# Kernel optimization log

Measured on AMD Instinct MI355X. Metric: run time of the kernel, lower is better.

## Reference

```python
import jax, jax.numpy as jnp
import numpy as np

GAMMA = 1.5
BN_EPS = 1e-5


def sparsemax(z):
    """Sparsemax along last axis (Martins & Astudillo, 2016)."""
    z = z - jnp.max(z, axis=-1, keepdims=True)
    z_sorted = -jnp.sort(-z, axis=-1)                      # descending sort
    z_cumsum = jnp.cumsum(z_sorted, axis=-1)
    k = jnp.arange(1, z.shape[-1] + 1, dtype=z.dtype)
    support = (z_sorted - (z_cumsum - 1.0) / k) > 0
    k_z = jnp.clip(jnp.sum(support, axis=-1, keepdims=True), 1, None).astype(z.dtype)
    idx = (k_z - 1.0).astype(jnp.int32)
    tau = (jnp.take_along_axis(z_cumsum, idx, axis=-1) - 1.0) / k_z
    return jnp.clip(z - tau, 0.0, None)


def setup_inputs() -> dict:
    key = jax.random.key(0)
    k1, k2 = jax.random.split(key)
    B, T, E, H = 32, 512, 512, 8
    x = jax.random.normal(k1, (B, T, E), dtype=jnp.float32)
    # torch Linear weight (out, in), kaiming-ish scale
    W = jax.random.normal(k2, (H, E, E), dtype=jnp.float32) / np.float32(np.sqrt(E))
    bn_weight = jnp.ones((H, E), dtype=jnp.float32)
    bn_bias = jnp.zeros((H, E), dtype=jnp.float32)
    return {"x": x, "W": W, "bn_weight": bn_weight, "bn_bias": bn_bias}


def reference(x, W, bn_weight, bn_bias):
    B, T, E = x.shape
    H = W.shape[0]
    gi = x.reshape(B * T, E)
    # all-head linear: y[n,o] = sum_i gi[n,i] * W[h,o,i]
    logits = jnp.einsum('ni,hoi->hno', gi, W)              # (H, B*T, E)
    # BatchNorm1d in training mode: batch stats over the B*T axis, biased var
    mean = jnp.mean(logits, axis=1, keepdims=True)
    var = jnp.var(logits, axis=1, keepdims=True)
    logits = (logits - mean) / jnp.sqrt(var + BN_EPS)
    logits = logits * bn_weight[:, None, :] + bn_bias[:, None, :]
    logits = logits.reshape(H, B, T, E)

    prior0 = jnp.ones((B, T, E), dtype=x.dtype)

    def step(prior, logits_h):
        mask_h = sparsemax(logits_h * prior)
        prior = prior * jnp.clip(GAMMA - mask_h, 0.0, None)
        return prior, mask_h

    _, masks = jax.lax.scan(step, prior0, logits)          # masks: (H, B, T, E)
    masked_xs = x[None, :, :, :] * masks                   # (H, B, T, E)
    return masked_xs, jnp.transpose(masks, (1, 0, 2, 3))   # (B, H, T, E)
```

## Files before the change

kernel.cpp:

```cpp
#include <hip/hip_runtime.h>
#include <stdint.h>

#define Hh 8
#define Bb 32
#define Tt 512
#define Ee 512
#define Nn 16384
#define GAMMA_ 1.5f
#define BN_EPS_ 1e-5f

typedef _Float16 f16x4 __attribute__((ext_vector_type(4)));
typedef _Float16 f16x8 __attribute__((ext_vector_type(8)));
typedef float    f32x4 __attribute__((ext_vector_type(4)));

__device__ __forceinline__ void async_ld16(void* lds, const void* g) {
    __builtin_amdgcn_global_load_lds(
        (const __attribute__((address_space(1))) void*)g,
        (__attribute__((address_space(3))) void*)lds, 16, 0, 0);
}

__device__ __forceinline__ float dpp_sum64(float v) {
    int t;
    t = __builtin_amdgcn_update_dpp(0, __float_as_int(v), 0x111, 0xf, 0xf, true);
    v += __int_as_float(t);
    t = __builtin_amdgcn_update_dpp(0, __float_as_int(v), 0x112, 0xf, 0xf, true);
    v += __int_as_float(t);
    t = __builtin_amdgcn_update_dpp(0, __float_as_int(v), 0x114, 0xf, 0xf, true);
    v += __int_as_float(t);
    t = __builtin_amdgcn_update_dpp(0, __float_as_int(v), 0x118, 0xf, 0xf, true);
    v += __int_as_float(t);
    t = __builtin_amdgcn_update_dpp(0, __float_as_int(v), 0x142, 0xf, 0xf, true);
    v += __int_as_float(t);
    t = __builtin_amdgcn_update_dpp(0, __float_as_int(v), 0x143, 0xf, 0xf, true);
    v += __int_as_float(t);
    return __int_as_float(__builtin_amdgcn_readlane(__float_as_int(v), 63));
}

__device__ __forceinline__ float dpp_max64(float v) {
    int t;
    t = __builtin_amdgcn_update_dpp(__float_as_int(v), __float_as_int(v), 0x111, 0xf, 0xf, false);
    v = fmaxf(v, __int_as_float(t));
    t = __builtin_amdgcn_update_dpp(__float_as_int(v), __float_as_int(v), 0x112, 0xf, 0xf, false);
    v = fmaxf(v, __int_as_float(t));
    t = __builtin_amdgcn_update_dpp(__float_as_int(v), __float_as_int(v), 0x114, 0xf, 0xf, false);
    v = fmaxf(v, __int_as_float(t));
    t = __builtin_amdgcn_update_dpp(__float_as_int(v), __float_as_int(v), 0x118, 0xf, 0xf, false);
    v = fmaxf(v, __int_as_float(t));
    t = __builtin_amdgcn_update_dpp(__float_as_int(v), __float_as_int(v), 0x142, 0xf, 0xf, false);
    v = fmaxf(v, __int_as_float(t));
    t = __builtin_amdgcn_update_dpp(__float_as_int(v), __float_as_int(v), 0x143, 0xf, 0xf, false);
    v = fmaxf(v, __int_as_float(t));
    return __int_as_float(__builtin_amdgcn_readlane(__float_as_int(v), 63));
}

__global__ __launch_bounds__(256) void cvt_kernel(const float* __restrict__ x,
                                                  const float* __restrict__ W,
                                                  _Float16* __restrict__ xh,
                                                  _Float16* __restrict__ wh,
                                                  float* __restrict__ sums) {
    const int NX = Bb * Tt * Ee;
    const int tid_g = blockIdx.x * 256 + threadIdx.x;
    int i = tid_g * 4;
    if (i < NX) {
        float4 v = *(const float4*)(x + i);
        f16x4 o = {(_Float16)v.x, (_Float16)v.y, (_Float16)v.z, (_Float16)v.w};
        *(f16x4*)(xh + i) = o;
    } else {
        int j = i - NX;
        float4 v = *(const float4*)(W + j);
        f16x4 o = {(_Float16)v.x, (_Float16)v.y, (_Float16)v.z, (_Float16)v.w};
        *(f16x4*)(wh + j) = o;
    }
    int zi = tid_g - (2621440 - 2048);
    if (zi >= 0) {
        float4 zz = {0.f, 0.f, 0.f, 0.f};
        ((float4*)sums)[zi] = zz;
    }
}

__global__ __launch_bounds__(512, 2) void gemm_kernel(const _Float16* __restrict__ A,
                                                      const _Float16* __restrict__ Bm,
                                                      _Float16* __restrict__ C,
                                                      float* __restrict__ sums,
                                                      float* __restrict__ sumsq) {
    __shared__ alignas(16) _Float16 As[2][256 * 32];
    __shared__ alignas(16) _Float16 Bs[2][256 * 32];
    const int id  = blockIdx.x;
    const int h   = id >> 7;
    const int rem = id & 127;
    const int mb  = (rem >> 1) * 256;
    const int nb  = (rem & 1) * 256;

    const int t    = threadIdx.x;
    const int lane = t & 63;
    const int w    = t >> 6;
    const int wrow = (w >> 2) * 128;
    const int wcol = (w & 3) * 64;
    const int quad = lane >> 4;
    const int l16  = lane & 15;

    const int kc = ((t & 3) - ((t >> 3) & 3)) & 3;
    const _Float16* Ap = A + (size_t)(mb + (t >> 2)) * Ee + kc * 8;
    const _Float16* Bp = Bm + (size_t)h * Ee * Ee + (size_t)(nb + (t >> 2)) * Ee + kc * 8;

    f32x4 acc[8][4] = {};

    async_ld16(&As[0][t * 8],        Ap);
    async_ld16(&As[0][4096 + t * 8], Ap + 128 * Ee);
    async_ld16(&Bs[0][t * 8],        Bp);
    async_ld16(&Bs[0][4096 + t * 8], Bp + 128 * Ee);

    const int so = ((quad + (l16 >> 1)) & 3) * 8;

    int buf = 0;
    for (int k0 = 0; k0 < Ee; k0 += 32) {
        __syncthreads();
        if (k0 + 32 < Ee) {
            int nx = buf ^ 1;
            async_ld16(&As[nx][t * 8],        Ap + k0 + 32);
            async_ld16(&As[nx][4096 + t * 8], Ap + 128 * Ee + k0 + 32);
            async_ld16(&Bs[nx][t * 8],        Bp + k0 + 32);
            async_ld16(&Bs[nx][4096 + t * 8], Bp + 128 * Ee + k0 + 32);
        }
        f16x8 b8[4];
#pragma unroll
        for (int nt = 0; nt < 4; ++nt)
            b8[nt] = *(const f16x8*)(&Bs[buf][(wcol + nt * 16 + l16) * 32 + so]);
#pragma unroll
        for (int mt = 0; mt < 8; ++mt) {
            f16x8 a8 = *(const f16x8*)(&As[buf][(wrow + mt * 16 + l16) * 32 + so]);
#pragma unroll
            for (int nt = 0; nt < 4; ++nt)
                acc[mt][nt] = __builtin_amdgcn_mfma_f32_16x16x32_f16(a8, b8[nt], acc[mt][nt], 0, 0, 0);
        }
        buf ^= 1;
    }

#pragma unroll
    for (int nt = 0; nt < 4; ++nt) {
        float sv = 0.f, ss = 0.f;
#pragma unroll
        for (int mt = 0; mt < 8; ++mt)
#pragma unroll
            for (int rr = 0; rr < 4; ++rr) { float v = acc[mt][nt][rr]; sv += v; ss += v * v; }
        sv += __shfl_xor(sv, 16, 64); sv += __shfl_xor(sv, 32, 64);
        ss += __shfl_xor(ss, 16, 64); ss += __shfl_xor(ss, 32, 64);
        if (quad == 0) {
            int col = nb + wcol + nt * 16 + l16;
            atomicAdd(&sums[h * Ee + col], sv);
            atomicAdd(&sumsq[h * Ee + col], ss);
        }
    }

    _Float16* Cp = C + (size_t)h * Nn * Ee;
#pragma unroll
    for (int mt = 0; mt < 8; ++mt)
#pragma unroll
        for (int rr = 0; rr < 4; ++rr) {
            int row = mb + wrow + mt * 16 + quad * 4 + rr;
            size_t off = (size_t)row * Ee + nb + wcol + l16;
#pragma unroll
            for (int nt = 0; nt < 4; ++nt)
                Cp[off + nt * 16] = (_Float16)acc[mt][nt][rr];
        }
}

__global__ __launch_bounds__(256) void stats_kernel(const float* __restrict__ sums,
                                                    const float* __restrict__ sumsq,
                                                    const float* __restrict__ bnw,
                                                    const float* __restrict__ bnb,
                                                    float* __restrict__ cA,
                                                    float* __restrict__ cB) {
    int i = blockIdx.x * 256 + threadIdx.x;
    float mean = sums[i] * (1.0f / Nn);
    float var  = sumsq[i] * (1.0f / Nn) - mean * mean;
    float inv  = rsqrtf(var + BN_EPS_);
    float a    = bnw[i] * inv;
    cA[i] = a;
    cB[i] = bnb[i] - mean * a;
}

__global__ __launch_bounds__(256) void rows_kernel(const float* __restrict__ x,
                                                   const _Float16* __restrict__ lg,
                                                   const float* __restrict__ cA,
                                                   const float* __restrict__ cB,
                                                   float* __restrict__ out) {
    const int n    = blockIdx.x * 4 + (threadIdx.x >> 6);
    const int lane = threadIdx.x & 63;
    const int e0   = lane * 4;
    const int bb   = n >> 9;
    const int tt   = n & 511;

    float xr[8], prior[8];
    {
        const float* xp = x + (size_t)n * Ee;
        float4 x0 = *(const float4*)(xp + e0);
        float4 x1 = *(const float4*)(xp + 256 + e0);
        xr[0]=x0.x; xr[1]=x0.y; xr[2]=x0.z; xr[3]=x0.w;
        xr[4]=x1.x; xr[5]=x1.y; xr[6]=x1.z; xr[7]=x1.w;
    }
#pragma unroll
    for (int j = 0; j < 8; ++j) prior[j] = 1.0f;

    float* omx = out;
    float* omk = out + (size_t)Hh * Nn * Ee;

    const _Float16* lrow = lg + (size_t)n * Ee;
    f16x4 l0 = *(const f16x4*)(lrow + e0);
    f16x4 l1 = *(const f16x4*)(lrow + 256 + e0);

#pragma unroll 1
    for (int h = 0; h < Hh; ++h) {
        f16x4 p0 = l0, p1 = l1;
        if (h + 1 < Hh) {
            const _Float16* lnx = lrow + (size_t)(h + 1) * Nn * Ee;
            p0 = *(const f16x4*)(lnx + e0);
            p1 = *(const f16x4*)(lnx + 256 + e0);
        }
        float z[8];
        {
            const float* ap = cA + h * Ee + e0;
            const float* bp = cB + h * Ee + e0;
            float4 a0 = *(const float4*)(ap);
            float4 b0 = *(const float4*)(bp);
            float4 a1 = *(const float4*)(ap + 256);
            float4 b1 = *(const float4*)(bp + 256);
            z[0] = ((float)l0[0] * a0.x + b0.x) * prior[0];
            z[1] = ((float)l0[1] * a0.y + b0.y) * prior[1];
            z[2] = ((float)l0[2] * a0.z + b0.z) * prior[2];
            z[3] = ((float)l0[3] * a0.w + b0.w) * prior[3];
            z[4] = ((float)l1[0] * a1.x + b1.x) * prior[4];
            z[5] = ((float)l1[1] * a1.y + b1.y) * prior[5];
            z[6] = ((float)l1[2] * a1.z + b1.z) * prior[6];
            z[7] = ((float)l1[3] * a1.w + b1.w) * prior[7];
        }

        float mx = z[0];
#pragma unroll
        for (int j = 1; j < 8; ++j) mx = fmaxf(mx, z[j]);
        float tau = dpp_max64(mx) - 1.0f;
        int cprev = -1;
#pragma unroll 1
        for (int it = 0; it < 64; ++it) {
            float s2 = 0.f;
            int cnt = 0;
#pragma unroll
            for (int j = 0; j < 8; ++j) {
                bool p = z[j] > tau;
                s2 += p ? z[j] : 0.0f;
                cnt += (int)__popcll(__ballot(p));
            }
            float S = dpp_sum64(s2);
            if (cnt == cprev) break;
            cprev = cnt;
            tau = (S - 1.0f) / (float)cnt;
        }

        size_t oxoff = ((size_t)h * Nn + n) * Ee + e0;
        size_t okoff = (((size_t)bb * Hh + h) * Tt + tt) * Ee + e0;
        f32x4 vx, vm;
#pragma unroll
        for (int j = 0; j < 4; ++j) {
            float m = fmaxf(z[j] - tau, 0.0f);
            prior[j] *= fmaxf(GAMMA_ - m, 0.0f);
            vm[j] = m; vx[j] = xr[j] * m;
        }
        __builtin_nontemporal_store(vx, (f32x4*)(omx + oxoff));
        __builtin_nontemporal_store(vm, (f32x4*)(omk + okoff));
#pragma unroll
        for (int j = 0; j < 4; ++j) {
            float m = fmaxf(z[4 + j] - tau, 0.0f);
            prior[4 + j] *= fmaxf(GAMMA_ - m, 0.0f);
            vm[j] = m; vx[j] = xr[4 + j] * m;
        }
        __builtin_nontemporal_store(vx, (f32x4*)(omx + oxoff + 256));
        __builtin_nontemporal_store(vm, (f32x4*)(omk + okoff + 256));
        l0 = p0; l1 = p1;
    }
}

extern "C" void kernel_launch(void* const* d_in, const int* in_sizes, int n_in,
                              void* d_out, int out_size, void* d_ws, size_t ws_size,
                              hipStream_t stream) {
    const float* x   = (const float*)d_in[0];
    const float* W   = (const float*)d_in[1];
    const float* bnw = (const float*)d_in[2];
    const float* bnb = (const float*)d_in[3];
    float* out = (float*)d_out;

    uint8_t* ws = (uint8_t*)d_ws;
    _Float16* xh = (_Float16*)(ws);
    _Float16* wh = (_Float16*)(ws + 16777216);
    _Float16* lg = (_Float16*)(ws + 20971520);
    float* sums  = (float*)(ws + 155189248);
    float* sumsq = (float*)(ws + 155205632);
    float* cA    = (float*)(ws + 155222016);
    float* cB    = (float*)(ws + 155238400);

    cvt_kernel<<<10240, 256, 0, stream>>>(x, W, xh, wh, sums);
    gemm_kernel<<<1024, 512, 0, stream>>>(xh, wh, lg, sums, sumsq);
    stats_kernel<<<16, 256, 0, stream>>>(sums, sumsq, bnw, bnb, cA, cB);
    rows_kernel<<<4096, 256, 0, stream>>>(x, lg, cA, cB, out);
}
```

Measured before the change: 646.3 us.

## Restructure GEMM mainloop into 8-phase ping-pong schedule with K=64 tiles

```diff
diff --git a/kernel.cpp b/kernel.cpp
--- a/kernel.cpp
+++ b/kernel.cpp
@@ -83,9 +83,9 @@
                                                       _Float16* __restrict__ C,
                                                       float* __restrict__ sums,
                                                       float* __restrict__ sumsq) {
-    __shared__ alignas(16) _Float16 As[2][256 * 32];
-    __shared__ alignas(16) _Float16 Bs[2][256 * 32];
-    const int id  = blockIdx.x;
+    __shared__ alignas(16) _Float16 As[2][256 * 64];
+    __shared__ alignas(16) _Float16 Bs[2][256 * 64];
+    const int id  = (blockIdx.x & 7) * 128 + (blockIdx.x >> 3);
     const int h   = id >> 7;
     const int rem = id & 127;
     const int mb  = (rem >> 1) * 256;
@@ -99,42 +99,123 @@
     const int quad = lane >> 4;
     const int l16  = lane & 15;
 
-    const int kc = ((t & 3) - ((t >> 3) & 3)) & 3;
-    const _Float16* Ap = A + (size_t)(mb + (t >> 2)) * Ee + kc * 8;
-    const _Float16* Bp = Bm + (size_t)h * Ee * Ee + (size_t)(nb + (t >> 2)) * Ee + kc * 8;
+    const int c = ((t & 7) - ((t >> 4) & 7)) & 7;
+    const _Float16* Ap = A + (size_t)(mb + (t >> 3)) * Ee + c * 8;
+    const _Float16* Bp = Bm + (size_t)h * Ee * Ee + (size_t)(nb + (t >> 3)) * Ee + c * 8;
+
+#define STG_A(b, q, tt) async_ld16(&As[b][(q) * 4096 + t * 8], Ap + (tt) * 64 + (q) * 64 * Ee)
+#define STG_B(b, q, tt) async_ld16(&Bs[b][(q) * 4096 + t * 8], Bp + (tt) * 64 + (q) * 64 * Ee)
+#define BAR() do { asm volatile("" ::: "memory"); __builtin_amdgcn_s_barrier(); \
+                   asm volatile("" ::: "memory"); } while (0)
 
     f32x4 acc[8][4] = {};
-
-    async_ld16(&As[0][t * 8],        Ap);
-    async_ld16(&As[0][4096 + t * 8], Ap + 128 * Ee);
-    async_ld16(&Bs[0][t * 8],        Bp);
-    async_ld16(&Bs[0][4096 + t * 8], Bp + 128 * Ee);
-
-    const int so = ((quad + (l16 >> 1)) & 3) * 8;
-
-    int buf = 0;
-    for (int k0 = 0; k0 < Ee; k0 += 32) {
-        __syncthreads();
-        if (k0 + 32 < Ee) {
-            int nx = buf ^ 1;
-            async_ld16(&As[nx][t * 8],        Ap + k0 + 32);
-            async_ld16(&As[nx][4096 + t * 8], Ap + 128 * Ee + k0 + 32);
-            async_ld16(&Bs[nx][t * 8],        Bp + k0 + 32);
-            async_ld16(&Bs[nx][4096 + t * 8], Bp + 128 * Ee + k0 + 32);
-        }
-        f16x8 b8[4];
-#pragma unroll
-        for (int nt = 0; nt < 4; ++nt)
-            b8[nt] = *(const f16x8*)(&Bs[buf][(wcol + nt * 16 + l16) * 32 + so]);
-#pragma unroll
-        for (int mt = 0; mt < 8; ++mt) {
-            f16x8 a8 = *(const f16x8*)(&As[buf][(wrow + mt * 16 + l16) * 32 + so]);
+    f16x8 a8[4], b8[2][4];
+
+    auto rdA = [&](int bsel, int mt, int kk) {
+        int row = wrow + mt * 16 + l16;
+        int sl  = ((kk * 4 + quad) + ((row >> 1) & 7)) & 7;
+        return *(const f16x8*)(&As[bsel][row * 64 + sl * 8]);
+    };
+    auto rdB = [&](int bsel, int nt, int kk) {
+        int row = wcol + nt * 16 + l16;
+        int sl  = ((kk * 4 + quad) + ((row >> 1) & 7)) & 7;
+        return *(const f16x8*)(&Bs[bsel][row * 64 + sl * 8]);
+    };
+    auto mm = [&](int mh, int kk) {
+        __builtin_amdgcn_s_setprio(1);
+#pragma unroll
+        for (int j = 0; j < 4; ++j)
 #pragma unroll
             for (int nt = 0; nt < 4; ++nt)
-                acc[mt][nt] = __builtin_amdgcn_mfma_f32_16x16x32_f16(a8, b8[nt], acc[mt][nt], 0, 0, 0);
-        }
-        buf ^= 1;
-    }
+                acc[mh * 4 + j][nt] = __builtin_amdgcn_mfma_f32_16x16x32_f16(
+                    a8[j], b8[kk][nt], acc[mh * 4 + j][nt], 0, 0, 0);
+        __builtin_amdgcn_s_setprio(0);
+    };
+
+#pragma unroll
+    for (int q = 0; q < 4; ++q) { STG_A(0, q, 0); STG_B(0, q, 0); }
+    STG_A(1, 0, 1); STG_A(1, 2, 1);
+    STG_B(1, 0, 1); STG_B(1, 1, 1); STG_B(1, 2, 1); STG_B(1, 3, 1);
+    asm volatile("s_waitcnt vmcnt(6)" ::: "memory");
+    BAR();
+
+#pragma unroll 1
+    for (int i = 0; i < 4; ++i) {
+        const int T1 = 2 * i + 1;
+        const int T2 = 2 * i + 2;
+        const int T3 = 2 * i + 3;
+        const bool st = (i < 3);
+
+#pragma unroll
+        for (int nt = 0; nt < 4; ++nt) b8[0][nt] = rdB(0, nt, 0);
+#pragma unroll
+        for (int j = 0; j < 4; ++j) a8[j] = rdA(0, j, 0);
+        STG_A(1, 1, T1); STG_A(1, 3, T1);
+        BAR();
+        mm(0, 0);
+        BAR();
+
+#pragma unroll
+        for (int nt = 0; nt < 4; ++nt) b8[1][nt] = rdB(0, nt, 1);
+#pragma unroll
+        for (int j = 0; j < 4; ++j) a8[j] = rdA(0, j, 1);
+        BAR();
+        mm(0, 1);
+        BAR();
+
+#pragma unroll
+        for (int j = 0; j < 4; ++j) a8[j] = rdA(0, 4 + j, 0);
+        if (st) { STG_A(0, 0, T2); STG_A(0, 2, T2); STG_B(0, 0, T2); STG_B(0, 1, T2); }
+        BAR();
+        mm(1, 0);
+        BAR();
+
+#pragma unroll
+        for (int j = 0; j < 4; ++j) a8[j] = rdA(0, 4 + j, 1);
+        if (st) { STG_B(0, 2, T2); STG_B(0, 3, T2); }
+        BAR();
+        mm(1, 1);
+        if (st) asm volatile("s_waitcnt vmcnt(6)" ::: "memory");
+        else    asm volatile("s_waitcnt vmcnt(0)" ::: "memory");
+        BAR();
+
+#pragma unroll
+        for (int nt = 0; nt < 4; ++nt) b8[0][nt] = rdB(1, nt, 0);
+#pragma unroll
+        for (int j = 0; j < 4; ++j) a8[j] = rdA(1, j, 0);
+        if (st) { STG_A(0, 1, T2); STG_A(0, 3, T2); }
+        BAR();
+        mm(0, 0);
+        BAR();
+
+#pragma unroll
+        for (int nt = 0; nt < 4; ++nt) b8[1][nt] = rdB(1, nt, 1);
+#pragma unroll
+        for (int j = 0; j < 4; ++j) a8[j] = rdA(1, j, 1);
+        BAR();
+        mm(0, 1);
+        BAR();
+
+#pragma unroll
+        for (int j = 0; j < 4; ++j) a8[j] = rdA(1, 4 + j, 0);
+        if (st) { STG_A(1, 0, T3); STG_A(1, 2, T3); STG_B(1, 0, T3); STG_B(1, 1, T3); }
+        BAR();
+        mm(1, 0);
+        BAR();
+
+#pragma unroll
+        for (int j = 0; j < 4; ++j) a8[j] = rdA(1, 4 + j, 1);
+        if (st) { STG_B(1, 2, T3); STG_B(1, 3, T3); }
+        BAR();
+        mm(1, 1);
+        if (st) {
+            asm volatile("s_waitcnt vmcnt(6)" ::: "memory");
+            BAR();
+        }
+    }
+#undef STG_A
+#undef STG_B
+#undef BAR
 
 #pragma unroll
     for (int nt = 0; nt < 4; ++nt) {
```

Measured after the change: 645.2 us (median of 2 runs). No clear change (-0.2%).
